# Kernel optimization log

Measured on AMD Instinct MI355X. Metric: run time of the kernel, lower is better.

Reference implementation:

```python
import jax, jax.numpy as jnp
import numpy as np

B, IN, H = 32768, 256, 256
CONCAT = IN + H

def _xavier(key, shape):
    fan_in, fan_out = shape
    limit = float(np.sqrt(6.0 / (fan_in + fan_out)))
    return jax.random.uniform(key, shape, jnp.float32, -limit, limit)

def setup_inputs() -> dict:
    key = jax.random.key(0)
    k = jax.random.split(key, 6)
    return {
        "x": jax.random.normal(k[0], (B, 1, IN), jnp.float32),
        "h_prev": jax.random.normal(k[1], (B, 1, H), jnp.float32),
        "wr": _xavier(k[2], (CONCAT, H)),
        "wz": _xavier(k[3], (CONCAT, H)),
        "whh": _xavier(k[4], (H, H)),
        "whx": _xavier(k[5], (IN, H)),
        "br": jnp.zeros((H,), jnp.float32),
        "bz": jnp.zeros((H,), jnp.float32),
        "bh": jnp.zeros((H,), jnp.float32),
    }

def reference(x, h_prev, wr, wz, whh, whx, br, bz, bh):
    # x: [B,1,IN], h_prev: [B,1,H]
    xc = jnp.concatenate([x, h_prev], axis=2)                  # [B,1,IN+H]
    r = jax.nn.sigmoid(jnp.matmul(xc, wr) + br)                # reset gate
    z = jax.nn.sigmoid(jnp.matmul(xc, wz) + bz)                # update gate
    g = jnp.tanh(jnp.matmul(r * h_prev, whh) + jnp.matmul(x, whx) + bh)
    h = (1 - z) * h_prev + z * g                               # gated blend
    return h
```

## Files before the change

kernel.cpp:

```cpp
#include <hip/hip_runtime.h>
#include <hip/hip_bf16.h>
#include <stdint.h>


typedef float  f32x4  __attribute__((ext_vector_type(4)));
typedef __bf16 bf16x8 __attribute__((ext_vector_type(8)));
typedef short  s16x8  __attribute__((ext_vector_type(8)));

#define B_TOT   32768
#define MT      64
#define WRZ_ELEMS (512*512)

__device__ __forceinline__ unsigned short f2b(float f) {
    union { float f; unsigned int u; } v; v.f = f;
    unsigned int r = (v.u + 0x7FFFu + ((v.u >> 16) & 1u)) >> 16;
    return (unsigned short)r;
}
__device__ __forceinline__ float b2f(unsigned short b) {
    union { unsigned int u; float f; } v; v.u = ((unsigned int)b) << 16;
    return v.f;
}
__device__ __forceinline__ ushort2 pk2(float a, float b) {
    __hip_bfloat162 t = __float22bfloat162_rn(make_float2(a, b));
    union { __hip_bfloat162 h; ushort2 u; } c; c.h = t; return c.u;
}
__device__ __forceinline__ float sigmoid_f(float x) {
    return 1.0f / (1.0f + __expf(-x));
}
__device__ __forceinline__ float tanh_f(float x) {
    return 1.0f - 2.0f / (__expf(2.0f * x) + 1.0f);
}

__device__ __forceinline__ int lds_idx(int row, int col) {
    return row * 512 + ((((col >> 3) ^ (row & 7)) << 3) | (col & 7));
}

__device__ __forceinline__ void stash8(unsigned short* dst, f32x4 a, f32x4 b) {
    union { ushort2 u2[4]; s16x8 v; } pk;
    pk.u2[0] = pk2(a[0], a[1]); pk.u2[1] = pk2(a[2], a[3]);
    pk.u2[2] = pk2(b[0], b[1]); pk.u2[3] = pk2(b[2], b[3]);
    *reinterpret_cast<s16x8*>(dst) = pk.v;
}

__device__ __forceinline__ f32x4 ldnt4(const float* p) {
    return __builtin_nontemporal_load(reinterpret_cast<const f32x4*>(p));
}

__global__ void prep_weights(const float* __restrict__ wr,
                             const float* __restrict__ wz,
                             const float* __restrict__ whh,
                             const float* __restrict__ whx,
                             unsigned short* __restrict__ wrz,
                             unsigned short* __restrict__ wg) {
    const int b = blockIdx.x;
    const int t = threadIdx.x;
    union { s16x8 v; unsigned short u[8]; } tmp;

    if (b < 128) {
        int w = b >> 4, ks = b & 15;
        int jn = t >> 6, l = t & 63;
        int kbase = ks * 32 + ((l >> 4) << 3);
        int n = 32 * w + ((jn & 1) << 4) + (l & 15);
        const float* src = (jn < 2) ? wr : wz;
        #pragma unroll
        for (int jj = 0; jj < 8; ++jj)
            tmp.u[jj] = f2b(src[(kbase + jj) * 256 + n]);
        *reinterpret_cast<s16x8*>(wrz + (size_t)w * 32768 + ks * 2048 + t * 8) = tmp.v;
    } else {
        int b2 = b - 128;
        int w = b2 >> 3, ksp = b2 & 7;
        int ksl = t >> 7, j = (t >> 6) & 1, l = t & 63;
        int ks = ksp * 2 + ksl;
        int kbase = ks * 32 + ((l >> 4) << 3);
        int n = 32 * w + (j << 4) + (l & 15);
        #pragma unroll
        for (int jj = 0; jj < 8; ++jj) {
            int k = kbase + jj;
            tmp.u[jj] = f2b((k < 256) ? whx[k * 256 + n] : whh[(k - 256) * 256 + n]);
        }
        *reinterpret_cast<s16x8*>(wg + (size_t)w * 16384 + ksp * 2048 + t * 8) = tmp.v;
    }
}

__global__ __launch_bounds__(512, 2)
void gru_fused(const float* __restrict__ x, const float* __restrict__ h,
               const unsigned short* __restrict__ wrz,
               const unsigned short* __restrict__ wg,
               const float* __restrict__ br, const float* __restrict__ bz,
               const float* __restrict__ bh, float* __restrict__ out) {
    __shared__ unsigned short xcA[64 * 512];

    const int tid  = threadIdx.x;
    const int lane = tid & 63;
    const int wv   = tid >> 6;
    const int m0   = lane & 15;
    const int q    = lane >> 4;
    const int rowBase = blockIdx.x * MT;

    float brv[2], bzv[2], bhv[2];
    #pragma unroll
    for (int j = 0; j < 2; ++j) {
        int col = 32 * wv + j * 16 + m0;
        brv[j] = br[col]; bzv[j] = bz[col]; bhv[j] = bh[col];
    }

    const int srow  = tid >> 3;
    const int scol8 = (tid & 7) << 3;
    const float* xrow = x + (size_t)(rowBase + srow) * 256 + scol8;
    const float* hrow = h + (size_t)(rowBase + srow) * 256 + scol8;

    const unsigned short* wrzP = wrz + (size_t)wv * 32768;
    const unsigned short* wgP  = wg  + (size_t)wv * 16384;

    f32x4 Sa[2], Sb[2];
    {
        Sa[0] = ldnt4(xrow);       Sb[0] = ldnt4(xrow + 4);
        Sa[1] = ldnt4(xrow + 64);  Sb[1] = ldnt4(xrow + 68);
    }

    s16x8 Bb[2][12];
    #pragma unroll
    for (int k2 = 0; k2 < 2; ++k2) {
        #pragma unroll
        for (int jn = 0; jn < 4; ++jn)
            Bb[0][k2 * 6 + jn] = *reinterpret_cast<const s16x8*>(
                wrzP + k2 * 2048 + jn * 512 + lane * 8);
        #pragma unroll
        for (int j = 0; j < 2; ++j)
            Bb[0][k2 * 6 + 4 + j] = *reinterpret_cast<const s16x8*>(
                wgP + k2 * 1024 + j * 512 + lane * 8);
    }

    stash8(&xcA[lds_idx(srow, scol8)], Sa[0], Sb[0]);
    asm volatile("s_waitcnt lgkmcnt(0)" ::: "memory");
    __builtin_amdgcn_sched_barrier(0);
    __builtin_amdgcn_s_barrier();
    __builtin_amdgcn_sched_barrier(0);

    f32x4 rz[4][4];
    f32x4 gac[2][4];
    #pragma unroll
    for (int jn = 0; jn < 4; ++jn)
        #pragma unroll
        for (int mt = 0; mt < 4; ++mt)
            rz[jn][mt] = (f32x4){0.f, 0.f, 0.f, 0.f};
    #pragma unroll
    for (int j = 0; j < 2; ++j)
        #pragma unroll
        for (int mt = 0; mt < 4; ++mt)
            gac[j][mt] = (f32x4){0.f, 0.f, 0.f, 0.f};

    #pragma unroll
    for (int grp = 0; grp < 8; ++grp) {
        const int cur = grp & 1, nxt = cur ^ 1;
        if (grp < 6) {
            const int s = grp + 2;
            const float* p = (s < 4) ? (xrow + 64 * s) : (hrow + 64 * (s - 4));
            Sa[grp & 1] = ldnt4(p); Sb[grp & 1] = ldnt4(p + 4);
        }
        if (grp < 7) {
            int gn = grp + 1;
            #pragma unroll
            for (int k2 = 0; k2 < 2; ++k2) {
                int ks = gn * 2 + k2;
                #pragma unroll
                for (int jn = 0; jn < 4; ++jn)
                    Bb[nxt][k2 * 6 + jn] = *reinterpret_cast<const s16x8*>(
                        wrzP + ks * 2048 + jn * 512 + lane * 8);
                if (gn < 4) {
                    #pragma unroll
                    for (int j = 0; j < 2; ++j)
                        Bb[nxt][k2 * 6 + 4 + j] = *reinterpret_cast<const s16x8*>(
                            wgP + ks * 1024 + j * 512 + lane * 8);
                }
            }
        }
        __builtin_amdgcn_sched_barrier(0);
        #pragma unroll
        for (int k2 = 0; k2 < 2; ++k2) {
            int ks = grp * 2 + k2;
            bf16x8 afr[4];
            #pragma unroll
            for (int mt = 0; mt < 4; ++mt) {
                int row = mt * 16 + m0;
                int idx = row * 512 + ((((ks << 2) | q) ^ (row & 7)) << 3);
                afr[mt] = __builtin_bit_cast(bf16x8,
                    *reinterpret_cast<const s16x8*>(&xcA[idx]));
            }
            #pragma unroll
            for (int jn = 0; jn < 4; ++jn) {
                bf16x8 bf = __builtin_bit_cast(bf16x8, Bb[cur][k2 * 6 + jn]);
                #pragma unroll
                for (int mt = 0; mt < 4; ++mt)
                    rz[jn][mt] = __builtin_amdgcn_mfma_f32_16x16x32_bf16(
                        afr[mt], bf, rz[jn][mt], 0, 0, 0);
            }
            if (grp < 4) {
                #pragma unroll
                for (int j = 0; j < 2; ++j) {
                    bf16x8 bf = __builtin_bit_cast(bf16x8, Bb[cur][k2 * 6 + 4 + j]);
                    #pragma unroll
                    for (int mt = 0; mt < 4; ++mt)
                        gac[j][mt] = __builtin_amdgcn_mfma_f32_16x16x32_bf16(
                            afr[mt], bf, gac[j][mt], 0, 0, 0);
                }
            }
        }
        __builtin_amdgcn_sched_barrier(0);
        if (grp < 7) {
            const int sb = (grp + 1) & 1;
            stash8(&xcA[lds_idx(srow, 64 * (grp + 1) + scol8)], Sa[sb], Sb[sb]);
            asm volatile("s_waitcnt lgkmcnt(0)" ::: "memory");
            __builtin_amdgcn_sched_barrier(0);
            __builtin_amdgcn_s_barrier();
            __builtin_amdgcn_sched_barrier(0);
        }
    }
    __syncthreads();

    s16x8 Tb[2][4];
    #pragma unroll
    for (int k2 = 0; k2 < 2; ++k2)
        #pragma unroll
        for (int j = 0; j < 2; ++j)
            Tb[0][k2 * 2 + j] = *reinterpret_cast<const s16x8*>(
                wgP + (8 + k2) * 1024 + j * 512 + lane * 8);

    #pragma unroll
    for (int j = 0; j < 2; ++j) {
        int col = 32 * wv + j * 16 + m0;
        #pragma unroll
        for (int mt = 0; mt < 4; ++mt) {
            #pragma unroll
            for (int rg = 0; rg < 4; ++rg) {
                int row = mt * 16 + q * 4 + rg;
                float hval = b2f(xcA[lds_idx(row, 256 + col)]);
                float rs = sigmoid_f(rz[j][mt][rg] + brv[j]);
                xcA[lds_idx(row, col)] = f2b(rs * hval);
                rz[j][mt][rg] = hval;
            }
        }
    }
    __syncthreads();

    #pragma unroll
    for (int tg = 0; tg < 4; ++tg) {
        const int cur = tg & 1, nxt = cur ^ 1;
        if (tg < 3) {
            #pragma unroll
            for (int k2 = 0; k2 < 2; ++k2)
                #pragma unroll
                for (int j = 0; j < 2; ++j)
                    Tb[nxt][k2 * 2 + j] = *reinterpret_cast<const s16x8*>(
                        wgP + (10 + tg * 2 + k2) * 1024 + j * 512 + lane * 8);
        }
        __builtin_amdgcn_sched_barrier(0);
        #pragma unroll
        for (int k2 = 0; k2 < 2; ++k2) {
            int kt = tg * 2 + k2;
            bf16x8 afr[4];
            #pragma unroll
            for (int mt = 0; mt < 4; ++mt) {
                int row = mt * 16 + m0;
                int idx = row * 512 + ((((kt << 2) | q) ^ (row & 7)) << 3);
                afr[mt] = __builtin_bit_cast(bf16x8,
                    *reinterpret_cast<const s16x8*>(&xcA[idx]));
            }
            #pragma unroll
            for (int j = 0; j < 2; ++j) {
                bf16x8 bf = __builtin_bit_cast(bf16x8, Tb[cur][k2 * 2 + j]);
                #pragma unroll
                for (int mt = 0; mt < 4; ++mt)
                    gac[j][mt] = __builtin_amdgcn_mfma_f32_16x16x32_bf16(
                        afr[mt], bf, gac[j][mt], 0, 0, 0);
            }
        }
    }

    #pragma unroll
    for (int j = 0; j < 2; ++j) {
        int col = 32 * wv + j * 16 + m0;
        #pragma unroll
        for (int mt = 0; mt < 4; ++mt) {
            #pragma unroll
            for (int rg = 0; rg < 4; ++rg) {
                int row = mt * 16 + q * 4 + rg;
                float zs = sigmoid_f(rz[2 + j][mt][rg] + bzv[j]);
                float gv = tanh_f(gac[j][mt][rg] + bhv[j]);
                float hval = rz[j][mt][rg];
                __builtin_nontemporal_store(hval + zs * (gv - hval),
                    out + (size_t)(rowBase + row) * 256 + col);
            }
        }
    }
}

extern "C" void kernel_launch(void* const* d_in, const int* in_sizes, int n_in,
                              void* d_out, int out_size, void* d_ws, size_t ws_size,
                              hipStream_t stream) {
    const float* x   = (const float*)d_in[0];
    const float* h   = (const float*)d_in[1];
    const float* wr  = (const float*)d_in[2];
    const float* wz  = (const float*)d_in[3];
    const float* whh = (const float*)d_in[4];
    const float* whx = (const float*)d_in[5];
    const float* br  = (const float*)d_in[6];
    const float* bz  = (const float*)d_in[7];
    const float* bh  = (const float*)d_in[8];
    float* out = (float*)d_out;

    unsigned short* wrz = (unsigned short*)d_ws;
    unsigned short* wg  = wrz + WRZ_ELEMS;

    prep_weights<<<192, 256, 0, stream>>>(wr, wz, whh, whx, wrz, wg);
    gru_fused<<<B_TOT / MT, 512, 0, stream>>>(x, h, wrz, wg, br, bz, bh, out);
}
```

Measured before the change: 154.6 us.

## Process two row tiles per block and prefetch next tile during epilogue

Each block now handles two 64-row tiles in sequence, halving the grid to 256 blocks. While the first tile runs its gate epilogue, the block prefetches the next tile's input and first weight fragments, hiding part of the prologue latency. The change also replaces divisions with hardware reciprocal in sigmoid and tanh, drops nontemporal load and store hints, and packs the r*h bf16 conversion two at a time. With 256 blocks on a GPU with about 256 CUs, occupancy per CU is lower and the tiles within a block run serially, so load balance and latency hiding may suffer.

```diff
diff --git a/kernel.cpp b/kernel.cpp
--- a/kernel.cpp
+++ b/kernel.cpp
@@ -25,10 +25,10 @@
     union { __hip_bfloat162 h; ushort2 u; } c; c.h = t; return c.u;
 }
 __device__ __forceinline__ float sigmoid_f(float x) {
-    return 1.0f / (1.0f + __expf(-x));
+    return __builtin_amdgcn_rcpf(1.0f + __expf(-x));
 }
 __device__ __forceinline__ float tanh_f(float x) {
-    return 1.0f - 2.0f / (__expf(2.0f * x) + 1.0f);
+    return 1.0f - 2.0f * __builtin_amdgcn_rcpf(__expf(2.0f * x) + 1.0f);
 }
 
 __device__ __forceinline__ int lds_idx(int row, int col) {
@@ -41,9 +41,8 @@
     pk.u2[2] = pk2(b[0], b[1]); pk.u2[3] = pk2(b[2], b[3]);
     *reinterpret_cast<s16x8*>(dst) = pk.v;
 }
-
-__device__ __forceinline__ f32x4 ldnt4(const float* p) {
-    return __builtin_nontemporal_load(reinterpret_cast<const f32x4*>(p));
+__device__ __forceinline__ f32x4 ld4(const float* p) {
+    return *reinterpret_cast<const f32x4*>(p);
 }
 
 __global__ void prep_weights(const float* __restrict__ wr,
@@ -95,7 +94,6 @@
     const int wv   = tid >> 6;
     const int m0   = lane & 15;
     const int q    = lane >> 4;
-    const int rowBase = blockIdx.x * MT;
 
     float brv[2], bzv[2], bhv[2];
     #pragma unroll
@@ -106,17 +104,15 @@
 
     const int srow  = tid >> 3;
     const int scol8 = (tid & 7) << 3;
-    const float* xrow = x + (size_t)(rowBase + srow) * 256 + scol8;
-    const float* hrow = h + (size_t)(rowBase + srow) * 256 + scol8;
+    const float* xrow0 = x + (size_t)(blockIdx.x * 2 * MT + srow) * 256 + scol8;
+    const float* hrow0 = h + (size_t)(blockIdx.x * 2 * MT + srow) * 256 + scol8;
 
     const unsigned short* wrzP = wrz + (size_t)wv * 32768;
     const unsigned short* wgP  = wg  + (size_t)wv * 16384;
 
     f32x4 Sa[2], Sb[2];
-    {
-        Sa[0] = ldnt4(xrow);       Sb[0] = ldnt4(xrow + 4);
-        Sa[1] = ldnt4(xrow + 64);  Sb[1] = ldnt4(xrow + 68);
-    }
+    Sa[0] = ld4(xrow0);       Sb[0] = ld4(xrow0 + 4);
+    Sa[1] = ld4(xrow0 + 64);  Sb[1] = ld4(xrow0 + 68);
 
     s16x8 Bb[2][12];
     #pragma unroll
@@ -131,74 +127,173 @@
                 wgP + k2 * 1024 + j * 512 + lane * 8);
     }
 
-    stash8(&xcA[lds_idx(srow, scol8)], Sa[0], Sb[0]);
-    asm volatile("s_waitcnt lgkmcnt(0)" ::: "memory");
-    __builtin_amdgcn_sched_barrier(0);
-    __builtin_amdgcn_s_barrier();
-    __builtin_amdgcn_sched_barrier(0);
-
-    f32x4 rz[4][4];
-    f32x4 gac[2][4];
     #pragma unroll
-    for (int jn = 0; jn < 4; ++jn)
-        #pragma unroll
-        for (int mt = 0; mt < 4; ++mt)
-            rz[jn][mt] = (f32x4){0.f, 0.f, 0.f, 0.f};
-    #pragma unroll
-    for (int j = 0; j < 2; ++j)
-        #pragma unroll
-        for (int mt = 0; mt < 4; ++mt)
-            gac[j][mt] = (f32x4){0.f, 0.f, 0.f, 0.f};
-
-    #pragma unroll
-    for (int grp = 0; grp < 8; ++grp) {
-        const int cur = grp & 1, nxt = cur ^ 1;
-        if (grp < 6) {
-            const int s = grp + 2;
-            const float* p = (s < 4) ? (xrow + 64 * s) : (hrow + 64 * (s - 4));
-            Sa[grp & 1] = ldnt4(p); Sb[grp & 1] = ldnt4(p + 4);
-        }
-        if (grp < 7) {
-            int gn = grp + 1;
+    for (int tile = 0; tile < 2; ++tile) {
+        const int rowBase = blockIdx.x * 2 * MT + tile * MT;
+        const float* xrow = xrow0 + tile * 16384;
+        const float* hrow = hrow0 + tile * 16384;
+
+        stash8(&xcA[lds_idx(srow, scol8)], Sa[0], Sb[0]);
+        asm volatile("s_waitcnt lgkmcnt(0)" ::: "memory");
+        __builtin_amdgcn_sched_barrier(0);
+        __builtin_amdgcn_s_barrier();
+        __builtin_amdgcn_sched_barrier(0);
+
+        f32x4 rz[4][4];
+        f32x4 gac[2][4];
+        #pragma unroll
+        for (int jn = 0; jn < 4; ++jn)
+            #pragma unroll
+            for (int mt = 0; mt < 4; ++mt)
+                rz[jn][mt] = (f32x4){0.f, 0.f, 0.f, 0.f};
+        #pragma unroll
+        for (int j = 0; j < 2; ++j)
+            #pragma unroll
+            for (int mt = 0; mt < 4; ++mt)
+                gac[j][mt] = (f32x4){0.f, 0.f, 0.f, 0.f};
+
+        #pragma unroll
+        for (int grp = 0; grp < 8; ++grp) {
+            const int cur = grp & 1, nxt = cur ^ 1;
+            if (grp < 6) {
+                const int s = grp + 2;
+                const float* p = (s < 4) ? (xrow + 64 * s) : (hrow + 64 * (s - 4));
+                Sa[grp & 1] = ld4(p); Sb[grp & 1] = ld4(p + 4);
+            }
+            if (grp < 7) {
+                int gn = grp + 1;
+                #pragma unroll
+                for (int k2 = 0; k2 < 2; ++k2) {
+                    int ks = gn * 2 + k2;
+                    #pragma unroll
+                    for (int jn = 0; jn < 4; ++jn)
+                        Bb[nxt][k2 * 6 + jn] = *reinterpret_cast<const s16x8*>(
+                            wrzP + ks * 2048 + jn * 512 + lane * 8);
+                    if (gn < 4) {
+                        #pragma unroll
+                        for (int j = 0; j < 2; ++j)
+                            Bb[nxt][k2 * 6 + 4 + j] = *reinterpret_cast<const s16x8*>(
+                                wgP + ks * 1024 + j * 512 + lane * 8);
+                    }
+                }
+            }
+            __builtin_amdgcn_sched_barrier(0);
             #pragma unroll
             for (int k2 = 0; k2 < 2; ++k2) {
-                int ks = gn * 2 + k2;
+                int ks = grp * 2 + k2;
+                bf16x8 afr[4];
+                #pragma unroll
+                for (int mt = 0; mt < 4; ++mt) {
+                    int row = mt * 16 + m0;
+                    int idx = row * 512 + ((((ks << 2) | q) ^ (row & 7)) << 3);
+                    afr[mt] = __builtin_bit_cast(bf16x8,
+                        *reinterpret_cast<const s16x8*>(&xcA[idx]));
+                }
+                #pragma unroll
+                for (int jn = 0; jn < 4; ++jn) {
+                    bf16x8 bf = __builtin_bit_cast(bf16x8, Bb[cur][k2 * 6 + jn]);
+                    #pragma unroll
+                    for (int mt = 0; mt < 4; ++mt)
+                        rz[jn][mt] = __builtin_amdgcn_mfma_f32_16x16x32_bf16(
+                            afr[mt], bf, rz[jn][mt], 0, 0, 0);
+                }
+                if (grp < 4) {
+                    #pragma unroll
+                    for (int j = 0; j < 2; ++j) {
+                        bf16x8 bf = __builtin_bit_cast(bf16x8, Bb[cur][k2 * 6 + 4 + j]);
+                        #pragma unroll
+                        for (int mt = 0; mt < 4; ++mt)
+                            gac[j][mt] = __builtin_amdgcn_mfma_f32_16x16x32_bf16(
+                                afr[mt], bf, gac[j][mt], 0, 0, 0);
+                    }
+                }
+            }
+            __builtin_amdgcn_sched_barrier(0);
+            if (grp < 7) {
+                const int sb = (grp + 1) & 1;
+                stash8(&xcA[lds_idx(srow, 64 * (grp + 1) + scol8)], Sa[sb], Sb[sb]);
+                asm volatile("s_waitcnt lgkmcnt(0)" ::: "memory");
+                __builtin_amdgcn_sched_barrier(0);
+                __builtin_amdgcn_s_barrier();
+                __builtin_amdgcn_sched_barrier(0);
+            }
+        }
+        __syncthreads();
+
+        s16x8 Tb[2][4];
+        #pragma unroll
+        for (int k2 = 0; k2 < 2; ++k2)
+            #pragma unroll
+            for (int j = 0; j < 2; ++j)
+                Tb[0][k2 * 2 + j] = *reinterpret_cast<const s16x8*>(
+                    wgP + (8 + k2) * 1024 + j * 512 + lane * 8);
+
+        if (tile == 0) {
+            const float* xn = xrow0 + 16384;
+            Sa[0] = ld4(xn);      Sb[0] = ld4(xn + 4);
+            Sa[1] = ld4(xn + 64); Sb[1] = ld4(xn + 68);
+            #pragma unroll
+            for (int k2 = 0; k2 < 2; ++k2) {
                 #pragma unroll
                 for (int jn = 0; jn < 4; ++jn)
-                    Bb[nxt][k2 * 6 + jn] = *reinterpret_cast<const s16x8*>(
-                        wrzP + ks * 2048 + jn * 512 + lane * 8);
-                if (gn < 4) {
+                    Bb[0][k2 * 6 + jn] = *reinterpret_cast<const s16x8*>(
+                        wrzP + k2 * 2048 + jn * 512 + lane * 8);
+                #pragma unroll
+                for (int j = 0; j < 2; ++j)
+                    Bb[0][k2 * 6 + 4 + j] = *reinterpret_cast<const s16x8*>(
+                        wgP + k2 * 1024 + j * 512 + lane * 8);
+            }
+        }
+
+        #pragma unroll
+        for (int j = 0; j < 2; ++j) {
+            int col = 32 * wv + j * 16 + m0;
+            #pragma unroll
+            for (int mt = 0; mt < 4; ++mt) {
+                #pragma unroll
+                for (int rg = 0; rg < 4; rg += 2) {
+                    int row0 = mt * 16 + q * 4 + rg;
+                    int row1 = row0 + 1;
+                    float h0 = b2f(xcA[lds_idx(row0, 256 + col)]);
+                    float h1 = b2f(xcA[lds_idx(row1, 256 + col)]);
+                    float a0 = sigmoid_f(rz[j][mt][rg]     + brv[j]) * h0;
+                    float a1 = sigmoid_f(rz[j][mt][rg + 1] + brv[j]) * h1;
+                    ushort2 c = pk2(a0, a1);
+                    xcA[lds_idx(row0, col)] = c.x;
+                    xcA[lds_idx(row1, col)] = c.y;
+                    rz[j][mt][rg]     = h0;
+                    rz[j][mt][rg + 1] = h1;
+                }
+            }
+        }
+        __syncthreads();
+
+        #pragma unroll
+        for (int tg = 0; tg < 4; ++tg) {
+            const int cur = tg & 1, nxt = cur ^ 1;
+            if (tg < 3) {
+                #pragma unroll
+                for (int k2 = 0; k2 < 2; ++k2)
                     #pragma unroll
                     for (int j = 0; j < 2; ++j)
-                        Bb[nxt][k2 * 6 + 4 + j] = *reinterpret_cast<const s16x8*>(
-                            wgP + ks * 1024 + j * 512 + lane * 8);
-                }
-            }
-        }
-        __builtin_amdgcn_sched_barrier(0);
-        #pragma unroll
-        for (int k2 = 0; k2 < 2; ++k2) {
-            int ks = grp * 2 + k2;
-            bf16x8 afr[4];
-            #pragma unroll
-            for (int mt = 0; mt < 4; ++mt) {
-                int row = mt * 16 + m0;
-                int idx = row * 512 + ((((ks << 2) | q) ^ (row & 7)) << 3);
-                afr[mt] = __builtin_bit_cast(bf16x8,
-                    *reinterpret_cast<const s16x8*>(&xcA[idx]));
-            }
-            #pragma unroll
-            for (int jn = 0; jn < 4; ++jn) {
-                bf16x8 bf = __builtin_bit_cast(bf16x8, Bb[cur][k2 * 6 + jn]);
-                #pragma unroll
-                for (int mt = 0; mt < 4; ++mt)
-                    rz[jn][mt] = __builtin_amdgcn_mfma_f32_16x16x32_bf16(
-                        afr[mt], bf, rz[jn][mt], 0, 0, 0);
-            }
-            if (grp < 4) {
+                        Tb[nxt][k2 * 2 + j] = *reinterpret_cast<const s16x8*>(
+                            wgP + (10 + tg * 2 + k2) * 1024 + j * 512 + lane * 8);
+            }
+            __builtin_amdgcn_sched_barrier(0);
+            #pragma unroll
+            for (int k2 = 0; k2 < 2; ++k2) {
+                int kt = tg * 2 + k2;
+                bf16x8 afr[4];
+                #pragma unroll
+                for (int mt = 0; mt < 4; ++mt) {
+                    int row = mt * 16 + m0;
+                    int idx = row * 512 + ((((kt << 2) | q) ^ (row & 7)) << 3);
+                    afr[mt] = __builtin_bit_cast(bf16x8,
+                        *reinterpret_cast<const s16x8*>(&xcA[idx]));
+                }
                 #pragma unroll
                 for (int j = 0; j < 2; ++j) {
-                    bf16x8 bf = __builtin_bit_cast(bf16x8, Bb[cur][k2 * 6 + 4 + j]);
+                    bf16x8 bf = __builtin_bit_cast(bf16x8, Tb[cur][k2 * 2 + j]);
                     #pragma unroll
                     for (int mt = 0; mt < 4; ++mt)
                         gac[j][mt] = __builtin_amdgcn_mfma_f32_16x16x32_bf16(
@@ -206,92 +301,25 @@
                 }
             }
         }
-        __builtin_amdgcn_sched_barrier(0);
-        if (grp < 7) {
-            const int sb = (grp + 1) & 1;
-            stash8(&xcA[lds_idx(srow, 64 * (grp + 1) + scol8)], Sa[sb], Sb[sb]);
-            asm volatile("s_waitcnt lgkmcnt(0)" ::: "memory");
-            __builtin_amdgcn_sched_barrier(0);
-            __builtin_amdgcn_s_barrier();
-            __builtin_amdgcn_sched_barrier(0);
-        }
-    }
-    __syncthreads();
-
-    s16x8 Tb[2][4];
-    #pragma unroll
-    for (int k2 = 0; k2 < 2; ++k2)
-        #pragma unroll
-        for (int j = 0; j < 2; ++j)
-            Tb[0][k2 * 2 + j] = *reinterpret_cast<const s16x8*>(
-                wgP + (8 + k2) * 1024 + j * 512 + lane * 8);
-
-    #pragma unroll
-    for (int j = 0; j < 2; ++j) {
-        int col = 32 * wv + j * 16 + m0;
-        #pragma unroll
-        for (int mt = 0; mt < 4; ++mt) {
-            #pragma unroll
-            for (int rg = 0; rg < 4; ++rg) {
-                int row = mt * 16 + q * 4 + rg;
-                float hval = b2f(xcA[lds_idx(row, 256 + col)]);
-                float rs = sigmoid_f(rz[j][mt][rg] + brv[j]);
-                xcA[lds_idx(row, col)] = f2b(rs * hval);
-                rz[j][mt][rg] = hval;
-            }
-        }
-    }
-    __syncthreads();
-
-    #pragma unroll
-    for (int tg = 0; tg < 4; ++tg) {
-        const int cur = tg & 1, nxt = cur ^ 1;
-        if (tg < 3) {
-            #pragma unroll
-            for (int k2 = 0; k2 < 2; ++k2)
-                #pragma unroll
-                for (int j = 0; j < 2; ++j)
-                    Tb[nxt][k2 * 2 + j] = *reinterpret_cast<const s16x8*>(
-                        wgP + (10 + tg * 2 + k2) * 1024 + j * 512 + lane * 8);
-        }
-        __builtin_amdgcn_sched_barrier(0);
-        #pragma unroll
-        for (int k2 = 0; k2 < 2; ++k2) {
-            int kt = tg * 2 + k2;
-            bf16x8 afr[4];
+
+        #pragma unroll
+        for (int j = 0; j < 2; ++j) {
+            int col = 32 * wv + j * 16 + m0;
             #pragma unroll
             for (int mt = 0; mt < 4; ++mt) {
-                int row = mt * 16 + m0;
-                int idx = row * 512 + ((((kt << 2) | q) ^ (row & 7)) << 3);
-                afr[mt] = __builtin_bit_cast(bf16x8,
-                    *reinterpret_cast<const s16x8*>(&xcA[idx]));
-            }
-            #pragma unroll
-            for (int j = 0; j < 2; ++j) {
-                bf16x8 bf = __builtin_bit_cast(bf16x8, Tb[cur][k2 * 2 + j]);
-                #pragma unroll
-                for (int mt = 0; mt < 4; ++mt)
-                    gac[j][mt] = __builtin_amdgcn_mfma_f32_16x16x32_bf16(
-                        afr[mt], bf, gac[j][mt], 0, 0, 0);
-            }
-        }
-    }
-
-    #pragma unroll
-    for (int j = 0; j < 2; ++j) {
-        int col = 32 * wv + j * 16 + m0;
-        #pragma unroll
-        for (int mt = 0; mt < 4; ++mt) {
-            #pragma unroll
-            for (int rg = 0; rg < 4; ++rg) {
-                int row = mt * 16 + q * 4 + rg;
-                float zs = sigmoid_f(rz[2 + j][mt][rg] + bzv[j]);
-                float gv = tanh_f(gac[j][mt][rg] + bhv[j]);
-                float hval = rz[j][mt][rg];
-                __builtin_nontemporal_store(hval + zs * (gv - hval),
-                    out + (size_t)(rowBase + row) * 256 + col);
-            }
-        }
+                #pragma unroll
+                for (int rg = 0; rg < 4; ++rg) {
+                    int row = mt * 16 + q * 4 + rg;
+                    float zs = sigmoid_f(rz[2 + j][mt][rg] + bzv[j]);
+                    float gv = tanh_f(gac[j][mt][rg] + bhv[j]);
+                    float hval = rz[j][mt][rg];
+                    out[(size_t)(rowBase + row) * 256 + col] = hval + zs * (gv - hval);
+                }
+            }
+        }
+
+        if (tile == 0)
+            __syncthreads();
     }
 }
 
@@ -313,5 +341,5 @@
     unsigned short* wg  = wrz + WRZ_ELEMS;
 
     prep_weights<<<192, 256, 0, stream>>>(wr, wz, whh, whx, wrz, wg);
-    gru_fused<<<B_TOT / MT, 512, 0, stream>>>(x, h, wrz, wg, br, bz, bh, out);
-}
+    gru_fused<<<B_TOT / (2 * MT), 512, 0, stream>>>(x, h, wrz, wg, br, bz, bh, out);
+}
```

New measurement: 185.9 us. 20.2% more time.
